# Kernel tuning notes

Hardware: AMD Instinct MI355X
Metric: run time of the kernel (lower is better)

## Reference

```python
import jax, jax.numpy as jnp
import numpy as np

B, N, D = 8, 16384, 256
WIDTH = 33
CENTER = 16


def setup_inputs() -> dict:
    key = jax.random.key(0)
    k1, k2, k3 = jax.random.split(key, 3)
    x = jax.random.normal(k1, (B, N, D), dtype=jnp.float32)
    # token sizes >= 1 (as produced by merging ones-initialized sizes)
    size = 1.0 + 4.0 * jax.random.uniform(k2, (B, N, 1), dtype=jnp.float32)
    # nonnegative window weights
    source_matrix = jax.random.uniform(k3, (B, N, WIDTH), dtype=jnp.float32)
    return {"x": x, "size": size, "source_matrix": source_matrix,
            "center": CENTER, "width": WIDTH}


def reference(x, size, source_matrix, center, width):
    # x: (B, N, d); size: (B, N, 1); source_matrix: (B, N, width)
    Bn, Nn, d = x.shape
    base = jnp.arange(Nn)

    def step(summed, off):
        pos = base + (off - center)                      # (N,)
        valid = (pos >= 0) & (pos < Nn)
        pc = jnp.clip(pos, 0, Nn - 1)
        gathered = x[:, pc, :]                           # (B, N, d)
        w = source_matrix[:, :, off] * valid.astype(x.dtype)  # (B, N)
        return summed + gathered * w[..., None], None

    summed, _ = jax.lax.scan(step, jnp.zeros_like(x), jnp.arange(width))
    denom = jnp.maximum(size, 1e-6)                      # (B, N, 1)
    return summed / denom
```

## Files before the change

kernel.cpp:

```cpp
#include <hip/hip_runtime.h>
#include <utility>

#define D_DIM 256
#define WID   33
#define CEN   16
#define RACC  4
#define XROWS (RACC + 2 * CEN)
#define RITER 16
#define NI    16
#define CHUNK (RITER * NI)
#define RING  64
#define PROL  48


typedef float f32x4 __attribute__((ext_vector_type(4)));

__device__ __forceinline__ float rdlane(float v, int l) {
    return __uint_as_float(__builtin_amdgcn_readlane(__float_as_uint(v), l));
}

__device__ __forceinline__ int clampN(int p, int N) {
    return p < 0 ? 0 : (p >= N ? N - 1 : p);
}

__device__ __forceinline__ f32x4 ld4(const float* p) {
    return *(const f32x4*)p;
}

__device__ __forceinline__ void dma_row(float* xs, int slot,
                                        const float* __restrict__ xlane,
                                        int row) {
    __builtin_amdgcn_global_load_lds(
        (const __attribute__((address_space(1))) void*)(xlane +
                                                        (size_t)row * D_DIM),
        (__attribute__((address_space(3))) void*)(xs + slot * D_DIM), 16, 0, 0);
}

template <size_t... Ss>
__device__ __forceinline__ void stage_prol(float* xs,
                                           const float* __restrict__ xlane,
                                           int base0, int N, int wv,
                                           std::index_sequence<Ss...>) {
    (([&] {
         const int s = wv * (PROL / 4) + (int)Ss;
         dma_row(xs, s, xlane, clampN(base0 + s, N));
     }()),
     ...);
}

__device__ __forceinline__ void stage_iter(float* xs,
                                           const float* __restrict__ xlane,
                                           int base0, int m, int N, int wv) {
#pragma unroll
    for (int kk = 0; kk < 4; ++kk) {
        const int k = wv * 4 + kk;
        const int s = (PROL + RITER * m + k) & (RING - 1);
        dma_row(xs, s, xlane, clampN(base0 + PROL + RITER * m + k, N));
    }
}

template <size_t... Rs>
__device__ __forceinline__ void load_w(float (&w)[RACC],
                                       const float* __restrict__ smb,
                                       int nbase, int minl, int N,
                                       std::index_sequence<Rs...>) {
    ((w[Rs] = smb[(size_t)clampN(nbase + (int)Rs, N) * WID + minl]), ...);
}

template <size_t... Rs>
__device__ __forceinline__ void zero_bad_w(float (&w)[RACC], int n0w, int lane,
                                           int N, std::index_sequence<Rs...>) {
    ((w[Rs] = ((unsigned)(n0w + (int)Rs - CEN + lane) < (unsigned)N)
                  ? w[Rs] : 0.0f),
     ...);
}

template <int J, size_t... Rs>
__device__ __forceinline__ void consume_j(f32x4 (&acc)[RACC],
                                          const float (&w)[RACC], f32x4 xv,
                                          std::index_sequence<Rs...>) {
    (([&] {
         constexpr int r = (int)Rs;
         if constexpr (J - r >= 0 && J - r < WID) {
             const float ws = rdlane(w[r], J - r);
             acc[r].x = fmaf(xv.x, ws, acc[r].x);
             acc[r].y = fmaf(xv.y, ws, acc[r].y);
             acc[r].z = fmaf(xv.z, ws, acc[r].z);
             acc[r].w = fmaf(xv.w, ws, acc[r].w);
         }
     }()),
     ...);
}

template <size_t... Js>
__device__ __forceinline__ void stream_rows(f32x4 (&acc)[RACC],
                                            const float (&w)[RACC],
                                            const float* xs, int sbase,
                                            int lane4,
                                            std::index_sequence<Js...>) {
    (([&] {
         const int s = (sbase + (int)Js) & (RING - 1);
         const f32x4 xv = ld4(xs + s * D_DIM + lane4);
         consume_j<(int)Js>(acc, w, xv, std::make_index_sequence<RACC>{});
     }()),
     ...);
}

template <size_t... Rs>
__device__ __forceinline__ void store_all(const f32x4 (&acc)[RACC], float szv,
                                          float* __restrict__ ob,
                                          std::index_sequence<Rs...>) {
    (([&] {
         constexpr int r = (int)Rs;
         const float inv = __builtin_amdgcn_rcpf(fmaxf(rdlane(szv, r), 1e-6f));
         f32x4 o;
         o.x = acc[r].x * inv; o.y = acc[r].y * inv;
         o.z = acc[r].z * inv; o.w = acc[r].w * inv;
         *(f32x4*)(ob + (size_t)r * D_DIM) = o;
     }()),
     ...);
}

__device__ __forceinline__ void iter_body(
    float* xs, const float* __restrict__ xlane, const float* __restrict__ smb,
    const float* __restrict__ szb, float* __restrict__ obl, int n0, int m,
    int N, int wv, int lane, int lane4, float (&wcur)[RACC],
    float (&wnxt)[RACC], float& szcur, float& sznxt, int minl) {
    if (m < NI - 1)
        stage_iter(xs, xlane, n0 - CEN, m, N, wv);
    __builtin_amdgcn_sched_barrier(0);
    const int n1 = n0 + RITER * (m + 1) + wv * RACC;
    load_w(wnxt, smb, n1, minl, N, std::make_index_sequence<RACC>{});
    sznxt = szb[clampN(n1 + (lane & 3), N)];
    __builtin_amdgcn_sched_barrier(0);

    const int n0w = n0 + RITER * m + wv * RACC;
    if (n0w < CEN || n0w + RACC - 1 + CEN >= N)
        zero_bad_w(wcur, n0w, lane, N, std::make_index_sequence<RACC>{});

    f32x4 acc[RACC] = {};
    stream_rows(acc, wcur, xs, RITER * m + wv * RACC, lane4,
                std::make_index_sequence<XROWS>{});
    store_all(acc, szcur, obl + (size_t)n0w * D_DIM,
              std::make_index_sequence<RACC>{});

    __syncthreads();
}

__global__ __launch_bounds__(256) void local_enc_kernel(
    const float* __restrict__ x, const float* __restrict__ sizev,
    const float* __restrict__ sm, float* __restrict__ out, int N) {
    __shared__ float xs[RING * D_DIM];

    const int bid   = blockIdx.x;
    const int swz   = (bid & 7) * 64 + (bid >> 3);
    const int strip = swz & 63;
    const int b     = swz >> 6;
    const int n0    = strip * CHUNK;
    const int tid   = threadIdx.x;
    const int wv    = tid >> 6;
    const int lane  = tid & 63;
    const int lane4 = lane * 4;

    const size_t bN = (size_t)b * (size_t)N;
    const float* __restrict__ xlane = x + bN * D_DIM + lane4;
    const float* __restrict__ smb   = sm + bN * WID;
    const float* __restrict__ szb   = sizev + bN;
    float* __restrict__ obl         = out + bN * D_DIM + lane4;

    stage_prol(xs, xlane, n0 - CEN, N, wv, std::make_index_sequence<PROL / 4>{});
    const int minl = (lane < WID) ? lane : (WID - 1);
    float wA[RACC], wB[RACC];
    float szA, szB;
    load_w(wA, smb, n0 + wv * RACC, minl, N, std::make_index_sequence<RACC>{});
    szA = szb[clampN(n0 + wv * RACC + (lane & 3), N)];
    __syncthreads();

#pragma unroll 1
    for (int mp = 0; mp < NI / 2; ++mp) {
        const int m0 = 2 * mp;
        iter_body(xs, xlane, smb, szb, obl, n0, m0, N, wv, lane, lane4,
                  wA, wB, szA, szB, minl);
        iter_body(xs, xlane, smb, szb, obl, n0, m0 + 1, N, wv, lane, lane4,
                  wB, wA, szB, szA, minl);
    }
}

extern "C" void kernel_launch(void* const* d_in, const int* in_sizes, int n_in,
                              void* d_out, int out_size, void* d_ws, size_t ws_size,
                              hipStream_t stream) {
    const float* x  = (const float*)d_in[0];
    const float* sz = (const float*)d_in[1];
    const float* sm = (const float*)d_in[2];
    float* out = (float*)d_out;

    const int B = 8;
    const int N = 16384;

    dim3 grid((N / CHUNK) * B, 1, 1);
    dim3 block(256, 1, 1);
    local_enc_kernel<<<grid, block, 0, stream>>>(x, sz, sm, out, N);
}
```

Before: 59.50 us.

## Split columns across wave pairs and double output rows per wave

Each wave now computes 8 output rows over half the feature columns (2 floats per lane) instead of 4 rows over all 256 columns (4 floats per lane). Each LDS row read then feeds 8 accumulators instead of 4, and the shared window of 2*CEN halo rows is amortised over more outputs, so fewer LDS bytes are read per FMA. In exchange, loads and stores shrink to 8-byte vectors, the weight and size broadcasts via readlane are duplicated across the two column-half waves, and the accumulator register count stays the same while the weight registers double.

```diff
diff --git a/kernel.cpp b/kernel.cpp
--- a/kernel.cpp
+++ b/kernel.cpp
@@ -4,7 +4,7 @@
 #define D_DIM 256
 #define WID   33
 #define CEN   16
-#define RACC  4
+#define RACC  8
 #define XROWS (RACC + 2 * CEN)
 #define RITER 16
 #define NI    16
@@ -13,7 +13,7 @@
 #define PROL  48
 
 
-typedef float f32x4 __attribute__((ext_vector_type(4)));
+typedef float f32x2 __attribute__((ext_vector_type(2)));
 
 __device__ __forceinline__ float rdlane(float v, int l) {
     return __uint_as_float(__builtin_amdgcn_readlane(__float_as_uint(v), l));
@@ -23,8 +23,8 @@
     return p < 0 ? 0 : (p >= N ? N - 1 : p);
 }
 
-__device__ __forceinline__ f32x4 ld4(const float* p) {
-    return *(const f32x4*)p;
+__device__ __forceinline__ f32x2 ld2(const float* p) {
+    return *(const f32x2*)p;
 }
 
 __device__ __forceinline__ void dma_row(float* xs, int slot,
@@ -76,8 +76,8 @@
 }
 
 template <int J, size_t... Rs>
-__device__ __forceinline__ void consume_j(f32x4 (&acc)[RACC],
-                                          const float (&w)[RACC], f32x4 xv,
+__device__ __forceinline__ void consume_j(f32x2 (&acc)[RACC],
+                                          const float (&w)[RACC], f32x2 xv,
                                           std::index_sequence<Rs...>) {
     (([&] {
          constexpr int r = (int)Rs;
@@ -85,38 +85,35 @@
              const float ws = rdlane(w[r], J - r);
              acc[r].x = fmaf(xv.x, ws, acc[r].x);
              acc[r].y = fmaf(xv.y, ws, acc[r].y);
-             acc[r].z = fmaf(xv.z, ws, acc[r].z);
-             acc[r].w = fmaf(xv.w, ws, acc[r].w);
          }
      }()),
      ...);
 }
 
 template <size_t... Js>
-__device__ __forceinline__ void stream_rows(f32x4 (&acc)[RACC],
+__device__ __forceinline__ void stream_rows(f32x2 (&acc)[RACC],
                                             const float (&w)[RACC],
                                             const float* xs, int sbase,
-                                            int lane4,
-                                            std::index_sequence<Js...>) {
+                                            int cp, std::index_sequence<Js...>) {
     (([&] {
          const int s = (sbase + (int)Js) & (RING - 1);
-         const f32x4 xv = ld4(xs + s * D_DIM + lane4);
+         const f32x2 xv = ld2(xs + s * D_DIM + cp);
          consume_j<(int)Js>(acc, w, xv, std::make_index_sequence<RACC>{});
      }()),
      ...);
 }
 
 template <size_t... Rs>
-__device__ __forceinline__ void store_all(const f32x4 (&acc)[RACC], float szv,
+__device__ __forceinline__ void store_all(const f32x2 (&acc)[RACC], float szv,
                                           float* __restrict__ ob,
                                           std::index_sequence<Rs...>) {
     (([&] {
          constexpr int r = (int)Rs;
          const float inv = __builtin_amdgcn_rcpf(fmaxf(rdlane(szv, r), 1e-6f));
-         f32x4 o;
-         o.x = acc[r].x * inv; o.y = acc[r].y * inv;
-         o.z = acc[r].z * inv; o.w = acc[r].w * inv;
-         *(f32x4*)(ob + (size_t)r * D_DIM) = o;
+         f32x2 o;
+         o.x = acc[r].x * inv;
+         o.y = acc[r].y * inv;
+         *(f32x2*)(ob + (size_t)r * D_DIM) = o;
      }()),
      ...);
 }
@@ -124,22 +121,22 @@
 __device__ __forceinline__ void iter_body(
     float* xs, const float* __restrict__ xlane, const float* __restrict__ smb,
     const float* __restrict__ szb, float* __restrict__ obl, int n0, int m,
-    int N, int wv, int lane, int lane4, float (&wcur)[RACC],
+    int N, int wv, int rg, int lane, int cp, float (&wcur)[RACC],
     float (&wnxt)[RACC], float& szcur, float& sznxt, int minl) {
     if (m < NI - 1)
         stage_iter(xs, xlane, n0 - CEN, m, N, wv);
     __builtin_amdgcn_sched_barrier(0);
-    const int n1 = n0 + RITER * (m + 1) + wv * RACC;
+    const int n1 = n0 + RITER * (m + 1) + rg * RACC;
     load_w(wnxt, smb, n1, minl, N, std::make_index_sequence<RACC>{});
-    sznxt = szb[clampN(n1 + (lane & 3), N)];
+    sznxt = szb[clampN(n1 + (lane & 7), N)];
     __builtin_amdgcn_sched_barrier(0);
 
-    const int n0w = n0 + RITER * m + wv * RACC;
+    const int n0w = n0 + RITER * m + rg * RACC;
     if (n0w < CEN || n0w + RACC - 1 + CEN >= N)
         zero_bad_w(wcur, n0w, lane, N, std::make_index_sequence<RACC>{});
 
-    f32x4 acc[RACC] = {};
-    stream_rows(acc, wcur, xs, RITER * m + wv * RACC, lane4,
+    f32x2 acc[RACC] = {};
+    stream_rows(acc, wcur, xs, RITER * m + rg * RACC, cp,
                 std::make_index_sequence<XROWS>{});
     store_all(acc, szcur, obl + (size_t)n0w * D_DIM,
               std::make_index_sequence<RACC>{});
@@ -160,28 +157,30 @@
     const int tid   = threadIdx.x;
     const int wv    = tid >> 6;
     const int lane  = tid & 63;
-    const int lane4 = lane * 4;
+    const int rg    = wv >> 1;
+    const int ch    = wv & 1;
+    const int cp    = ch * 128 + lane * 2;
 
     const size_t bN = (size_t)b * (size_t)N;
-    const float* __restrict__ xlane = x + bN * D_DIM + lane4;
+    const float* __restrict__ xlane = x + bN * D_DIM + lane * 4;
     const float* __restrict__ smb   = sm + bN * WID;
     const float* __restrict__ szb   = sizev + bN;
-    float* __restrict__ obl         = out + bN * D_DIM + lane4;
+    float* __restrict__ obl         = out + bN * D_DIM + cp;
 
     stage_prol(xs, xlane, n0 - CEN, N, wv, std::make_index_sequence<PROL / 4>{});
     const int minl = (lane < WID) ? lane : (WID - 1);
     float wA[RACC], wB[RACC];
     float szA, szB;
-    load_w(wA, smb, n0 + wv * RACC, minl, N, std::make_index_sequence<RACC>{});
-    szA = szb[clampN(n0 + wv * RACC + (lane & 3), N)];
+    load_w(wA, smb, n0 + rg * RACC, minl, N, std::make_index_sequence<RACC>{});
+    szA = szb[clampN(n0 + rg * RACC + (lane & 7), N)];
     __syncthreads();
 
 #pragma unroll 1
     for (int mp = 0; mp < NI / 2; ++mp) {
         const int m0 = 2 * mp;
-        iter_body(xs, xlane, smb, szb, obl, n0, m0, N, wv, lane, lane4,
+        iter_body(xs, xlane, smb, szb, obl, n0, m0, N, wv, rg, lane, cp,
                   wA, wB, szA, szB, minl);
-        iter_body(xs, xlane, smb, szb, obl, n0, m0 + 1, N, wv, lane, lane4,
+        iter_body(xs, xlane, smb, szb, obl, n0, m0 + 1, N, wv, rg, lane, cp,
                   wB, wA, szB, szA, minl);
     }
 }
```

Result: slower. 65.65 us (+10.3%).

## Stage x tiles in LDS as bf16 via register loads, halve chunk size

Applied to the files above, without the earlier changes.

Replaces direct global-to-LDS DMA with register loads that convert x to bf16 before writing to shared memory, halving the LDS footprint and LDS read bandwidth per row. Staging now loads into registers early and writes after compute, and chunk size halves so the grid doubles. This lowers accuracy of x to bf16 (accumulation stays fp32), which may exceed tolerance, and adds conversion ALU work and register pressure.

```diff
diff --git a/kernel.cpp b/kernel.cpp
--- a/kernel.cpp
+++ b/kernel.cpp
@@ -7,10 +7,11 @@
 #define RACC  4
 #define XROWS (RACC + 2 * CEN)
 #define RITER 16
-#define NI    16
+#define NI    8
 #define CHUNK (RITER * NI)
 #define RING  64
 #define PROL  48
+#define LROW  128
 
 
 typedef float f32x4 __attribute__((ext_vector_type(4)));
@@ -27,36 +28,56 @@
     return *(const f32x4*)p;
 }
 
-__device__ __forceinline__ void dma_row(float* xs, int slot,
-                                        const float* __restrict__ xlane,
-                                        int row) {
-    __builtin_amdgcn_global_load_lds(
-        (const __attribute__((address_space(1))) void*)(xlane +
-                                                        (size_t)row * D_DIM),
-        (__attribute__((address_space(3))) void*)(xs + slot * D_DIM), 16, 0, 0);
+__device__ __forceinline__ unsigned bfbits(float f) {
+    __bf16 b = (__bf16)f;
+    return (unsigned)__builtin_bit_cast(unsigned short, b);
+}
+
+__device__ __forceinline__ uint2 pack4(f32x4 v) {
+    uint2 r;
+    r.x = (bfbits(v.y) << 16) | bfbits(v.x);
+    r.y = (bfbits(v.w) << 16) | bfbits(v.z);
+    return r;
+}
+
+__device__ __forceinline__ f32x4 unpack4(uint2 d) {
+    f32x4 v;
+    v.x = __uint_as_float(d.x << 16);
+    v.y = __uint_as_float(d.x & 0xffff0000u);
+    v.z = __uint_as_float(d.y << 16);
+    v.w = __uint_as_float(d.y & 0xffff0000u);
+    return v;
 }
 
 template <size_t... Ss>
-__device__ __forceinline__ void stage_prol(float* xs,
-                                           const float* __restrict__ xlane,
-                                           int base0, int N, int wv,
+__device__ __forceinline__ void stage_prol(unsigned* xs,
+                                           const float* __restrict__ xgl,
+                                           int base0, int N, int wv, int lane2,
                                            std::index_sequence<Ss...>) {
     (([&] {
          const int s = wv * (PROL / 4) + (int)Ss;
-         dma_row(xs, s, xlane, clampN(base0 + s, N));
-     }()),
-     ...);
-}
-
-__device__ __forceinline__ void stage_iter(float* xs,
-                                           const float* __restrict__ xlane,
-                                           int base0, int m, int N, int wv) {
-#pragma unroll
-    for (int kk = 0; kk < 4; ++kk) {
-        const int k = wv * 4 + kk;
-        const int s = (PROL + RITER * m + k) & (RING - 1);
-        dma_row(xs, s, xlane, clampN(base0 + PROL + RITER * m + k, N));
-    }
+         const int p = clampN(base0 + s, N);
+         *(uint2*)(xs + s * LROW + lane2) = pack4(ld4(xgl + (size_t)p * D_DIM));
+     }()),
+     ...);
+}
+
+template <size_t... Ks>
+__device__ __forceinline__ void stage_load(f32x4 (&sv)[RACC],
+                                           const float* __restrict__ xgl,
+                                           int rowb, int N, int wv,
+                                           std::index_sequence<Ks...>) {
+    ((sv[Ks] = ld4(xgl + (size_t)clampN(rowb + wv * 4 + (int)Ks, N) * D_DIM)),
+     ...);
+}
+
+template <size_t... Ks>
+__device__ __forceinline__ void stage_write(unsigned* xs, const f32x4 (&sv)[RACC],
+                                            int slotb, int wv, int lane2,
+                                            std::index_sequence<Ks...>) {
+    ((*(uint2*)(xs + ((slotb + wv * 4 + (int)Ks) & (RING - 1)) * LROW + lane2) =
+          pack4(sv[Ks])),
+     ...);
 }
 
 template <size_t... Rs>
@@ -95,13 +116,14 @@
 template <size_t... Js>
 __device__ __forceinline__ void stream_rows(f32x4 (&acc)[RACC],
                                             const float (&w)[RACC],
-                                            const float* xs, int sbase,
-                                            int lane4,
+                                            const unsigned* xs, int sbase,
+                                            int lane2,
                                             std::index_sequence<Js...>) {
     (([&] {
          const int s = (sbase + (int)Js) & (RING - 1);
-         const f32x4 xv = ld4(xs + s * D_DIM + lane4);
-         consume_j<(int)Js>(acc, w, xv, std::make_index_sequence<RACC>{});
+         const uint2 d = *(const uint2*)(xs + s * LROW + lane2);
+         consume_j<(int)Js>(acc, w, unpack4(d),
+                            std::make_index_sequence<RACC>{});
      }()),
      ...);
 }
@@ -122,12 +144,15 @@
 }
 
 __device__ __forceinline__ void iter_body(
-    float* xs, const float* __restrict__ xlane, const float* __restrict__ smb,
+    unsigned* xs, const float* __restrict__ xgl, const float* __restrict__ smb,
     const float* __restrict__ szb, float* __restrict__ obl, int n0, int m,
-    int N, int wv, int lane, int lane4, float (&wcur)[RACC],
+    int N, int wv, int lane, int lane2, float (&wcur)[RACC],
     float (&wnxt)[RACC], float& szcur, float& sznxt, int minl) {
-    if (m < NI - 1)
-        stage_iter(xs, xlane, n0 - CEN, m, N, wv);
+    f32x4 sv[RACC];
+    const bool more = (m < NI - 1);
+    if (more)
+        stage_load(sv, xgl, n0 - CEN + PROL + RITER * m, N, wv,
+                   std::make_index_sequence<RACC>{});
     __builtin_amdgcn_sched_barrier(0);
     const int n1 = n0 + RITER * (m + 1) + wv * RACC;
     load_w(wnxt, smb, n1, minl, N, std::make_index_sequence<RACC>{});
@@ -139,36 +164,42 @@
         zero_bad_w(wcur, n0w, lane, N, std::make_index_sequence<RACC>{});
 
     f32x4 acc[RACC] = {};
-    stream_rows(acc, wcur, xs, RITER * m + wv * RACC, lane4,
+    stream_rows(acc, wcur, xs, RITER * m + wv * RACC, lane2,
                 std::make_index_sequence<XROWS>{});
     store_all(acc, szcur, obl + (size_t)n0w * D_DIM,
               std::make_index_sequence<RACC>{});
 
+    if (more)
+        stage_write(xs, sv, PROL + RITER * m, wv, lane2,
+                    std::make_index_sequence<RACC>{});
+
     __syncthreads();
 }
 
 __global__ __launch_bounds__(256) void local_enc_kernel(
     const float* __restrict__ x, const float* __restrict__ sizev,
     const float* __restrict__ sm, float* __restrict__ out, int N) {
-    __shared__ float xs[RING * D_DIM];
+    __shared__ unsigned xs[RING * LROW];
 
     const int bid   = blockIdx.x;
-    const int swz   = (bid & 7) * 64 + (bid >> 3);
-    const int strip = swz & 63;
-    const int b     = swz >> 6;
+    const int swz   = (bid & 7) * 128 + (bid >> 3);
+    const int strip = swz & 127;
+    const int b     = swz >> 7;
     const int n0    = strip * CHUNK;
     const int tid   = threadIdx.x;
     const int wv    = tid >> 6;
     const int lane  = tid & 63;
     const int lane4 = lane * 4;
+    const int lane2 = lane * 2;
 
     const size_t bN = (size_t)b * (size_t)N;
-    const float* __restrict__ xlane = x + bN * D_DIM + lane4;
-    const float* __restrict__ smb   = sm + bN * WID;
-    const float* __restrict__ szb   = sizev + bN;
-    float* __restrict__ obl         = out + bN * D_DIM + lane4;
-
-    stage_prol(xs, xlane, n0 - CEN, N, wv, std::make_index_sequence<PROL / 4>{});
+    const float* __restrict__ xgl = x + bN * D_DIM + lane4;
+    const float* __restrict__ smb = sm + bN * WID;
+    const float* __restrict__ szb = sizev + bN;
+    float* __restrict__ obl       = out + bN * D_DIM + lane4;
+
+    stage_prol(xs, xgl, n0 - CEN, N, wv, lane2,
+               std::make_index_sequence<PROL / 4>{});
     const int minl = (lane < WID) ? lane : (WID - 1);
     float wA[RACC], wB[RACC];
     float szA, szB;
@@ -179,9 +210,9 @@
 #pragma unroll 1
     for (int mp = 0; mp < NI / 2; ++mp) {
         const int m0 = 2 * mp;
-        iter_body(xs, xlane, smb, szb, obl, n0, m0, N, wv, lane, lane4,
+        iter_body(xs, xgl, smb, szb, obl, n0, m0, N, wv, lane, lane2,
                   wA, wB, szA, szB, minl);
-        iter_body(xs, xlane, smb, szb, obl, n0, m0 + 1, N, wv, lane, lane4,
+        iter_body(xs, xgl, smb, szb, obl, n0, m0 + 1, N, wv, lane, lane2,
                   wB, wA, szB, szA, minl);
     }
 }
```

New measurement: 63.46 us. 6.6% more time.
